# Performance work log

Measured on AMD Instinct MI355X. Metric: run time of the kernel, lower is better.

Reference implementation:

```python
import jax, jax.numpy as jnp
import numpy as np

B, N, H = 8, 2000, 64  # batch, num_nodes(=input_dim), hidden(num_gru_units)


def _laplacian_self_loop(a):
    # batched: norm = D^{-1/2} (A + I) D^{-1/2}
    m = a + jnp.eye(a.shape[-1], dtype=a.dtype)
    d_inv_sqrt = jnp.sum(m, axis=-1) ** -0.5  # (B, N)
    return d_inv_sqrt[..., :, None] * m * d_inv_sqrt[..., None, :]


def _graph_conv(inputs, hidden_flat, adj, windd, W2, b2, W3, b3, W, b, out_dim):
    b_, _, n = inputs.shape
    # dynamic wind-based adjacency
    wind_now = inputs[:, 2, :] * 360.0  # (B, N)
    direction = jnp.abs(windd[None, :, :] - wind_now[:, :, None])  # (B, N, N)
    direction = jnp.where(direction > 360.0, 180.0, direction)
    d1 = jnp.maximum(jnp.cos(direction * (jnp.pi / 180.0)), 0.0)
    a = d1 @ W2.T + b2 + (adj @ W3.T + b3)[None]  # (B, N, N)
    a1 = _laplacian_self_loop(jnp.maximum(a, 0.0))
    # graph conv: concat [x, h] then A @ [.] then Linear
    x = jnp.concatenate([inputs[:, 0, :, None], hidden_flat.reshape(b_, n, H)], axis=2)  # (B,N,H+1)
    y = jnp.einsum('bij,bjh->bih', a1, x) @ W.T + b  # (B, N, out_dim)
    return y.reshape(b_, n * out_dim)


def reference(inputs, hidden_state, adj, windd, W2, b2, W3, b3, W1a, b1a, W1b, b1b, Wca1, Wca2, Wsa):
    b_, _, n = inputs.shape
    conc = _graph_conv(inputs, hidden_state, adj, windd, W2, b2, W3, b3, W1a, b1a, 2 * H)
    conc = conc.reshape(b_, 2 * H, n)  # faithful reshape (input_dim == N)
    # --- channel attention (CBAM) ---
    avg = jnp.mean(conc, axis=2, keepdims=True)  # (B, 2H, 1)
    mx = jnp.max(conc, axis=2, keepdims=True)
    def fc(v):
        return jnp.einsum('oc,bcx->box', Wca2, jax.nn.relu(jnp.einsum('oc,bcx->box', Wca1, v)))
    ca = jax.nn.sigmoid(fc(avg) + fc(mx))  # (B, 2H, 1)
    conc = ca * conc
    # --- spatial attention ---
    s = jnp.stack([jnp.mean(conc, axis=1), jnp.max(conc, axis=1)], axis=1)  # (B, 2, N)
    sa = jax.lax.conv_general_dilated(s, Wsa, window_strides=(1,), padding=((3, 3),),
                                      dimension_numbers=('NCH', 'OIH', 'NCH'))  # (B,1,N)
    conc = jax.nn.sigmoid(sa) * conc
    # --- GRU gates ---
    conc = jax.nn.sigmoid(conc.reshape(b_, 2 * H * n))
    r, u = jnp.split(conc, 2, axis=1)  # each (B, N*H)
    c = jnp.tanh(_graph_conv(inputs, r * hidden_state, adj, windd, W2, b2, W3, b3, W1b, b1b, H))
    new_hidden_state = u * hidden_state + (1.0 - u) * c
    return new_hidden_state


def setup_inputs() -> dict:
    key = jax.random.key(0)
    ks = jax.random.split(key, 12)
    inputs = jax.random.uniform(ks[0], (B, 3, N), dtype=jnp.float32)
    hidden_state = jax.random.normal(ks[1], (B, N * H), dtype=jnp.float32) * 0.1
    adj = jax.random.uniform(ks[2], (N, N), dtype=jnp.float32)
    windd = jax.random.uniform(ks[3], (N, N), dtype=jnp.float32) * 360.0
    sN = 1.0 / np.sqrt(N)
    W2 = jax.random.normal(ks[4], (N, N), dtype=jnp.float32) * sN
    b2 = jnp.zeros((N,), jnp.float32)
    W3 = jax.random.normal(ks[5], (N, N), dtype=jnp.float32) * sN
    b3 = jnp.zeros((N,), jnp.float32)
    sI = 1.0 / np.sqrt(H + 1)
    W1a = jax.random.normal(ks[6], (2 * H, H + 1), dtype=jnp.float32) * sI
    b1a = jnp.ones((2 * H,), jnp.float32)  # bias=1.0 in graph_conv1
    W1b = jax.random.normal(ks[7], (H, H + 1), dtype=jnp.float32) * sI
    b1b = jnp.zeros((H,), jnp.float32)
    Wca1 = jax.random.normal(ks[8], (2 * H // 16, 2 * H), dtype=jnp.float32) * (1.0 / np.sqrt(2 * H))
    Wca2 = jax.random.normal(ks[9], (2 * H, 2 * H // 16), dtype=jnp.float32) * (1.0 / np.sqrt(2 * H // 16))
    Wsa = jax.random.normal(ks[10], (1, 2, 7), dtype=jnp.float32) * (1.0 / np.sqrt(14))
    return {'inputs': inputs, 'hidden_state': hidden_state, 'adj': adj, 'windd': windd,
            'W2': W2, 'b2': b2, 'W3': W3, 'b3': b3, 'W1a': W1a, 'b1a': b1a,
            'W1b': W1b, 'b1b': b1b, 'Wca1': Wca1, 'Wca2': Wca2, 'Wsa': Wsa}
```

## Files before the change

kernel.cpp:

```cpp
#include <hip/hip_runtime.h>

#define NN 2000
#define BB 8
#define P  2048
#define NIT 32

typedef __attribute__((ext_vector_type(8))) short bf16x8;
typedef __attribute__((ext_vector_type(4))) float f32x4;

__device__ __forceinline__ float sigf(float x) { return 1.0f / (1.0f + expf(-x)); }

__device__ __forceinline__ short f2bf(float x) {
    union { float f; unsigned u; } v; v.f = x;
    unsigned r = v.u + 0x7fffu + ((v.u >> 16) & 1u);
    return (short)(r >> 16);
}
__device__ __forceinline__ float bf2f(short h) {
    union { unsigned u; float f; } v; v.u = ((unsigned)(unsigned short)h) << 16; return v.f;
}

__device__ __forceinline__ void gl2lds16(const short* g, short* l) {
    __builtin_amdgcn_global_load_lds(
        (const __attribute__((address_space(1))) void*)g,
        (__attribute__((address_space(3))) void*)l, 16, 0, 0);
}

__global__ __launch_bounds__(256) void k_cvt(
    const float* __restrict__ W2, const float* __restrict__ W3,
    const float* __restrict__ adj, const float* __restrict__ windd,
    const float* __restrict__ inputs,
    short* __restrict__ W2bf, short* __restrict__ W3bf,
    short* __restrict__ adjbf, short* __restrict__ d1bf)
{
    const int i = blockIdx.x, sel = blockIdx.y, t = threadIdx.x;
    const bool live = (i < NN) && (t < 250);
    if (sel < 3) {
        const float* s = (sel == 0) ? W2 : (sel == 1) ? W3 : adj;
        short* d = ((sel == 0) ? W2bf : (sel == 1) ? W3bf : adjbf) + ((size_t)i) * P + t * 8;
        bf16x8 v;
#pragma unroll
        for (int e = 0; e < 8; ++e) v[e] = 0;
        if (live) {
            const float* p = s + (size_t)i * NN + t * 8;
            float4 x0 = *(const float4*)p;
            float4 x1 = *(const float4*)(p + 4);
            float a[8] = {x0.x,x0.y,x0.z,x0.w,x1.x,x1.y,x1.z,x1.w};
#pragma unroll
            for (int e = 0; e < 8; ++e) v[e] = f2bf(a[e]);
        }
        *(bf16x8*)d = v;
    } else {
        const float DEG = 0.01745329251994329577f;
        float cw[8], sw[8];
        if (live) {
            const float* p = windd + (size_t)i * NN + t * 8;
            float4 x0 = *(const float4*)p;
            float4 x1 = *(const float4*)(p + 4);
            float a[8] = {x0.x,x0.y,x0.z,x0.w,x1.x,x1.y,x1.z,x1.w};
#pragma unroll
            for (int e = 0; e < 8; ++e) {
                float r = a[e] * DEG;
                cw[e] = __cosf(r);
                sw[e] = __sinf(r);
            }
        }
        __shared__ float cwn[8], swn[8];
        if (t < 8 && i < NN) {
            float wn = inputs[(size_t)t * 3 * NN + 2 * NN + i] * (360.0f * DEG);
            cwn[t] = __cosf(wn);
            swn[t] = __sinf(wn);
        }
        __syncthreads();
#pragma unroll
        for (int b = 0; b < BB; ++b) {
            bf16x8 v;
#pragma unroll
            for (int e = 0; e < 8; ++e) v[e] = 0;
            if (live) {
                const float cb_ = cwn[b], sb_ = swn[b];
#pragma unroll
                for (int e = 0; e < 8; ++e)
                    v[e] = f2bf(fmaxf(fmaf(cw[e], cb_, sw[e] * sb_), 0.0f));
            }
            *(bf16x8*)(d1bf + ((size_t)b * P + i) * P + t * 8) = v;
        }
    }
}

__global__ __launch_bounds__(512, 2) void k_gd(
    const short* __restrict__ d1bf, const short* __restrict__ W2bf,
    const float* __restrict__ b2, const short* __restrict__ adjw,
    short* __restrict__ m_bf, float* __restrict__ rowpart)
{
    __shared__ char smem[131072];
    const int t = threadIdx.x;
    const int w = t >> 6, lane = t & 63;
    const int wm = w >> 2, wn = w & 3;
    const int lr = lane & 15, lq = lane >> 4;
    const int tile = blockIdx.x;
    const int b = blockIdx.y;
    const int i0 = (tile & 7) * 256;
    const int j0 = (tile >> 3) * 256;
    const short* A  = d1bf + (size_t)b * P * P;
    const short* Bm = W2bf;

    const short* srcA[4];
    const short* srcB[4];
#pragma unroll
    for (int q = 0; q < 4; ++q) {
        const int c = q * 512 + t;
        const int r = c >> 3;
        const int g = (c & 7) ^ (r & 7);
        srcA[q] = A  + (size_t)(i0 + r) * P + g * 8;
        srcB[q] = Bm + (size_t)(j0 + r) * P + g * 8;
    }

#define STAGE_ALL(slot, ktI) do {                                                      \
        gl2lds16(srcA[0] + (ktI) * 64, (short*)(smem + (slot) * 32768 + (w * 64) * 16));          \
        gl2lds16(srcA[1] + (ktI) * 64, (short*)(smem + (slot) * 32768 + (512 + w * 64) * 16));    \
        gl2lds16(srcA[2] + (ktI) * 64, (short*)(smem + (slot) * 32768 + (1024 + w * 64) * 16));   \
        gl2lds16(srcA[3] + (ktI) * 64, (short*)(smem + (slot) * 32768 + (1536 + w * 64) * 16));   \
        gl2lds16(srcB[0] + (ktI) * 64, (short*)(smem + 65536 + (slot) * 32768 + (w * 64) * 16));          \
        gl2lds16(srcB[1] + (ktI) * 64, (short*)(smem + 65536 + (slot) * 32768 + (512 + w * 64) * 16));    \
        gl2lds16(srcB[2] + (ktI) * 64, (short*)(smem + 65536 + (slot) * 32768 + (1024 + w * 64) * 16));   \
        gl2lds16(srcB[3] + (ktI) * 64, (short*)(smem + 65536 + (slot) * 32768 + (1536 + w * 64) * 16)); } while (0)

    const int fx0 = (lq << 4) ^ ((lr & 7) << 4);
    const int fx1 = ((4 + lq) << 4) ^ ((lr & 7) << 4);
    const int arowB = (wm * 128 + lr) * 128;
    const int browB = (wn * 64 + lr) * 128;

    f32x4 acc[8][4];
#pragma unroll
    for (int m = 0; m < 8; ++m)
#pragma unroll
        for (int n = 0; n < 4; ++n) acc[m][n] = (f32x4){0.f, 0.f, 0.f, 0.f};
    bf16x8 aF[4][2], bF[4][2];

    STAGE_ALL(0, 0);
    asm volatile("s_waitcnt vmcnt(0)" ::: "memory");
    __builtin_amdgcn_s_barrier();
    asm volatile("" ::: "memory");

#define MFMA_(a_, b_, m, n) acc[m][n] = __builtin_amdgcn_mfma_f32_16x16x32_bf16(a_, b_, acc[m][n], 0, 0, 0)

    for (int kt = 0; kt < NIT; ++kt) {
        char* curA = smem + (kt & 1) * 32768;
        char* curB = smem + 65536 + (kt & 1) * 32768;
        const int stgSlot = (kt + 1) & 1;
        const int stgKt = (kt + 1 < NIT) ? (kt + 1) : (NIT - 1);

        STAGE_ALL(stgSlot, stgKt);

#pragma unroll
        for (int m = 0; m < 4; ++m) {
            aF[m][0] = *(const bf16x8*)(curA + arowB + m * 2048 + fx0);
            aF[m][1] = *(const bf16x8*)(curA + arowB + m * 2048 + fx1);
        }
#pragma unroll
        for (int n = 0; n < 4; ++n) {
            bF[n][0] = *(const bf16x8*)(curB + browB + n * 2048 + fx0);
            bF[n][1] = *(const bf16x8*)(curB + browB + n * 2048 + fx1);
        }
        asm volatile("s_waitcnt lgkmcnt(0)" ::: "memory");
        __builtin_amdgcn_sched_barrier(0);
        __builtin_amdgcn_s_setprio(1);
#pragma unroll
        for (int m = 0; m < 4; ++m)
#pragma unroll
            for (int n = 0; n < 4; ++n) {
                MFMA_(aF[m][0], bF[n][0], m, n);
                MFMA_(aF[m][1], bF[n][1], m, n);
            }
        __builtin_amdgcn_s_setprio(0);

#pragma unroll
        for (int m = 0; m < 4; ++m) {
            aF[m][0] = *(const bf16x8*)(curA + arowB + (m + 4) * 2048 + fx0);
            aF[m][1] = *(const bf16x8*)(curA + arowB + (m + 4) * 2048 + fx1);
        }
        asm volatile("s_waitcnt lgkmcnt(0)" ::: "memory");
        __builtin_amdgcn_sched_barrier(0);
        __builtin_amdgcn_s_setprio(1);
#pragma unroll
        for (int m = 0; m < 4; ++m)
#pragma unroll
            for (int n = 0; n < 4; ++n) {
                MFMA_(aF[m][0], bF[n][0], m + 4, n);
                MFMA_(aF[m][1], bF[n][1], m + 4, n);
            }
        __builtin_amdgcn_s_setprio(0);

        asm volatile("s_waitcnt vmcnt(0)" ::: "memory");
        __builtin_amdgcn_s_barrier();
        asm volatile("" ::: "memory");
    }

    const int rbase = i0 + wm * 128 + lq * 4;
    const int cbase = j0 + wn * 64 + lr;
    float* red = (float*)smem;
#pragma unroll
    for (int m = 0; m < 8; ++m) {
#pragma unroll
        for (int q = 0; q < 4; ++q) {
            const int row = rbase + m * 16 + q;
            float rs = 0.0f;
#pragma unroll
            for (int n = 0; n < 4; ++n) {
                const int col = cbase + n * 16;
                short o = 0;
                if (row < NN && col < NN) {
                    float x = acc[m][n][q] + b2[col] + bf2f(adjw[(size_t)row * NN + col]);
                    x = fmaxf(x, 0.0f);
                    if (row == col) x += 1.0f;
                    o = f2bf(x);
                    rs += x;
                }
                m_bf[((size_t)b * P + row) * P + col] = o;
            }
            red[(wm * 128 + m * 16 + lq * 4 + q) * 66 + (wn * 16 + lr)] = rs;
        }
    }
    __syncthreads();
    if (t < 256) {
        const float* rr = red + t * 66;
        float s = 0.0f;
#pragma unroll
        for (int k2 = 0; k2 < 64; ++k2) s += rr[k2];
        const int row = i0 + t;
        if (row < NN)
            rowpart[((size_t)b * 8 + (tile >> 3)) * 2048 + row] = s;
    }
#undef MFMA_
#undef STAGE_ALL
}

template<int EPI>
__global__ __launch_bounds__(256) void k_mfma(
    const short* __restrict__ Abase, const short* __restrict__ Bbase,
    const float* __restrict__ bias,
    void* __restrict__ Cout, short* __restrict__ part, size_t aBatch)
{
    __shared__ short shA[4096];
    __shared__ short shB[4096];
    const int t = threadIdx.x;
    const int w = t >> 6, lane = t & 63;
    const int wr = w >> 1, wc = w & 1;

    int i0, j0, b, kt = 0;
    if (EPI == 2) {
        i0 = blockIdx.x * 128; j0 = 0; kt = blockIdx.y; b = blockIdx.z;
    } else {
        i0 = blockIdx.x * 128; j0 = blockIdx.y * 128; b = 0;
    }
    const int kb = (EPI == 2) ? kt * (P / 4) : 0;
    const int ke = (EPI == 2) ? kt * (P / 4) + (P / 4) : P;

    const short* A  = Abase + (size_t)b * aBatch;
    const short* Bm = Bbase + ((EPI == 2) ? (size_t)b * 128 * P : (size_t)0);

    f32x4 acc[4][4];
#pragma unroll
    for (int m = 0; m < 4; ++m)
#pragma unroll
        for (int n = 0; n < 4; ++n) acc[m][n] = (f32x4){0.f, 0.f, 0.f, 0.f};

    const int lidx0 = w * 128 + lane;
    const int lidx1 = lidx0 + 64;
    const int rA0 = lidx0 >> 2, rA1 = lidx1 >> 2;
    const int gA0 = (lidx0 & 3) ^ ((lidx0 >> 3) & 3);
    const int gA1 = (lidx1 & 3) ^ ((lidx1 >> 3) & 3);
    const short* aS0 = A  + (size_t)(i0 + rA0) * P + gA0 * 8;
    const short* aS1 = A  + (size_t)(i0 + rA1) * P + gA1 * 8;
    const short* bS0 = Bm + (size_t)(j0 + rA0) * P + gA0 * 8;
    const short* bS1 = Bm + (size_t)(j0 + rA1) * P + gA1 * 8;
    short* ldA0 = shA + lidx0 * 8 - lane * 8 + lane * 8;
    short* ldA1 = shA + lidx1 * 8;
    short* ldB0 = shB + lidx0 * 8;
    short* ldB1 = shB + lidx1 * 8;

    const int lr = lane & 15, lq = lane >> 4;
    const int axr = (lq ^ ((lr >> 1) & 3)) << 3;
    const int aoff = (wr * 64 + lr) * 32 + axr;
    const int boff = (wc * 64 + lr) * 32 + axr;

    for (int k0 = kb; k0 < ke; k0 += 32) {
        gl2lds16(aS0 + k0, ldA0);
        gl2lds16(aS1 + k0, ldA1);
        gl2lds16(bS0 + k0, ldB0);
        gl2lds16(bS1 + k0, ldB1);
        __syncthreads();
        bf16x8 aF[4], bF[4];
#pragma unroll
        for (int m = 0; m < 4; ++m) aF[m] = *(const bf16x8*)(shA + aoff + m * 512);
#pragma unroll
        for (int n = 0; n < 4; ++n) bF[n] = *(const bf16x8*)(shB + boff + n * 512);
#pragma unroll
        for (int m = 0; m < 4; ++m)
#pragma unroll
            for (int n = 0; n < 4; ++n)
                acc[m][n] = __builtin_amdgcn_mfma_f32_16x16x32_bf16(aF[m], bF[n], acc[m][n], 0, 0, 0);
        __syncthreads();
    }

    const int rbase = i0 + wr * 64 + lq * 4;
    const int cbase = j0 + wc * 64 + lr;
#pragma unroll
    for (int m = 0; m < 4; ++m) {
#pragma unroll
        for (int n = 0; n < 4; ++n) {
            const int col = cbase + n * 16;
#pragma unroll
            for (int q = 0; q < 4; ++q) {
                const int row = rbase + m * 16 + q;
                float v = acc[m][n][q];
                if (EPI == 0) {
                    if (row < NN && col < NN)
                        ((short*)Cout)[(size_t)row * NN + col] = f2bf(v + bias[col]);
                } else {
                    if (row < NN && col < 128)
                        part[((size_t)(kt * BB + b) * NN + row) * 128 + col] = f2bf(v);
                }
            }
        }
    }
}

__global__ __launch_bounds__(256) void k_agg64(
    const short* __restrict__ m_bf, const short* __restrict__ zT,
    short* __restrict__ part)
{
    __shared__ short shA[4096];
    __shared__ short shB[2048];
    const int t = threadIdx.x;
    const int w = t >> 6, lane = t & 63;
    const int wr = w >> 1, wc = w & 1;
    const int i0 = blockIdx.x * 128;
    const int kt = blockIdx.y, b = blockIdx.z;
    const int kb = kt * (P / 4), ke = kb + (P / 4);
    const short* A  = m_bf + (size_t)b * P * P;
    const short* Bm = zT + (size_t)b * 128 * P;

    f32x4 acc[4][2];
#pragma unroll
    for (int m = 0; m < 4; ++m)
#pragma unroll
        for (int n = 0; n < 2; ++n) acc[m][n] = (f32x4){0.f, 0.f, 0.f, 0.f};

    const int lidx0 = w * 128 + lane;
    const int lidx1 = lidx0 + 64;
    const int gA0 = (lidx0 & 3) ^ ((lidx0 >> 3) & 3);
    const int gA1 = (lidx1 & 3) ^ ((lidx1 >> 3) & 3);
    const int gB  = (t & 3) ^ ((t >> 3) & 3);
    const short* aS0 = A  + (size_t)(i0 + (lidx0 >> 2)) * P + gA0 * 8;
    const short* aS1 = A  + (size_t)(i0 + (lidx1 >> 2)) * P + gA1 * 8;
    const short* bS  = Bm + (size_t)(t >> 2) * P + gB * 8;
    short* ldA0 = shA + lidx0 * 8;
    short* ldA1 = shA + lidx1 * 8;
    short* ldB  = shB + t * 8;

    const int lr = lane & 15, lq = lane >> 4;
    const int axr = (lq ^ ((lr >> 1) & 3)) << 3;
    const int aoff = (wr * 64 + lr) * 32 + axr;
    const int boff = (wc * 32 + lr) * 32 + axr;

    for (int k0 = kb; k0 < ke; k0 += 32) {
        gl2lds16(aS0 + k0, ldA0);
        gl2lds16(aS1 + k0, ldA1);
        gl2lds16(bS + k0, ldB);
        __syncthreads();
        bf16x8 aF[4], bF[2];
#pragma unroll
        for (int m = 0; m < 4; ++m) aF[m] = *(const bf16x8*)(shA + aoff + m * 512);
#pragma unroll
        for (int n = 0; n < 2; ++n) bF[n] = *(const bf16x8*)(shB + boff + n * 512);
#pragma unroll
        for (int m = 0; m < 4; ++m)
#pragma unroll
            for (int n = 0; n < 2; ++n)
                acc[m][n] = __builtin_amdgcn_mfma_f32_16x16x32_bf16(aF[m], bF[n], acc[m][n], 0, 0, 0);
        __syncthreads();
    }

    const int rbase = i0 + wr * 64 + lq * 4;
    const int cbase = wc * 32 + lr;
#pragma unroll
    for (int m = 0; m < 4; ++m) {
#pragma unroll
        for (int n = 0; n < 2; ++n) {
            const int col = cbase + n * 16;
#pragma unroll
            for (int q = 0; q < 4; ++q) {
                const int row = rbase + m * 16 + q;
                if (row < NN)
                    part[((size_t)(kt * BB + b) * NN + row) * 64 + col] = f2bf(acc[m][n][q]);
            }
        }
    }
}

__global__ __launch_bounds__(256) void k_combred(
    const short* __restrict__ part, const float* __restrict__ dinv,
    const float* __restrict__ bias, float* __restrict__ conc,
    float* __restrict__ avg, float* __restrict__ mx)
{
    const int c = blockIdx.x, b = blockIdx.y, t = threadIdx.x;
    const size_t S = (size_t)BB * NN * 128;
    const size_t base = (size_t)b * NN * 128;
    float sm = 0.0f, sx = -3.402823466e+38f;
    for (int n = t; n < NN; n += 256) {
        const size_t f = (size_t)c * NN + n;
        const int i = (int)(f >> 7), o = (int)(f & 127);
        const size_t pidx = base + f;
        float s = (bf2f(part[pidx]) + bf2f(part[pidx + S])) +
                  (bf2f(part[pidx + 2 * S]) + bf2f(part[pidx + 3 * S]));
        float v = s * dinv[b * NN + i] + bias[o];
        conc[pidx] = v;
        sm += v; sx = fmaxf(sx, v);
    }
#pragma unroll
    for (int off = 32; off > 0; off >>= 1) {
        sm += __shfl_down(sm, off);
        sx = fmaxf(sx, __shfl_down(sx, off));
    }
    __shared__ float rs[4], rm[4];
    if ((t & 63) == 0) { rs[t >> 6] = sm; rm[t >> 6] = sx; }
    __syncthreads();
    if (t == 0) {
        avg[b * 128 + c] = (rs[0] + rs[1] + rs[2] + rs[3]) * (1.0f / NN);
        mx[b * 128 + c]  = fmaxf(fmaxf(rm[0], rm[1]), fmaxf(rm[2], rm[3]));
    }
}

__global__ __launch_bounds__(256) void k_cfin(
    const short* __restrict__ part, const float* __restrict__ dinv,
    const float* __restrict__ bias, const float* __restrict__ u,
    const float* __restrict__ hidden, float* __restrict__ out)
{
    const size_t idx = (size_t)blockIdx.x * 256 + threadIdx.x;
    const size_t S = (size_t)BB * NN * 64;
    if (idx >= S) return;
    const int o = (int)(idx & 63);
    const size_t r = idx >> 6;
    const int i = (int)(r % NN);
    const int b = (int)(r / NN);
    float s = (bf2f(part[idx]) + bf2f(part[idx + S])) +
              (bf2f(part[idx + 2 * S]) + bf2f(part[idx + 3 * S]));
    float c = tanhf(s * dinv[b * NN + i] + bias[o]);
    float uu = u[idx];
    out[idx] = uu * hidden[idx] + (1.0f - uu) * c;
}

template<int OUT>
__global__ __launch_bounds__(128) void k_xwT(
    const float* __restrict__ inputs, const float* __restrict__ hsrc,
    const float* __restrict__ W, const float* __restrict__ rowpart,
    float* __restrict__ dinv, short* __restrict__ zT)
{
    const int b = blockIdx.y;
    const int j0 = blockIdx.x * 16;
    const int t = threadIdx.x;
    __shared__ float wl[128 * 65];
    __shared__ float xs[16 * 66];
    __shared__ float dj[16];
    for (int idx = t; idx < OUT * 65; idx += 128) wl[idx] = W[idx];
    for (int idx = t; idx < 16 * 64; idx += 128) {
        int jj = idx >> 6, hh = idx & 63, j = j0 + jj;
        xs[jj * 66 + 1 + hh] = (j < NN) ? hsrc[((size_t)b * NN + j) * 64 + hh] : 0.0f;
    }
    if (t < 16) {
        int j = j0 + t;
        xs[t * 66] = (j < NN) ? inputs[(size_t)b * 3 * NN + j] : 0.0f;
        float dv = 0.0f;
        if (j < NN) {
            if (OUT == 128) {
                float s = 0.0f;
#pragma unroll
                for (int jt = 0; jt < 8; ++jt)
                    s += rowpart[((size_t)b * 8 + jt) * 2048 + j];
                dv = rsqrtf(s);
                dinv[b * NN + j] = dv;
            } else {
                dv = dinv[b * NN + j];
            }
        }
        dj[t] = dv;
    }
    __syncthreads();
    for (int jj = 0; jj < 16; ++jj) {
        float a = 0.0f;
        if (t < OUT) {
            const float* xr = &xs[jj * 66];
            const float* wr = &wl[t * 65];
#pragma unroll
            for (int c = 0; c < 65; ++c) a = fmaf(xr[c], wr[c], a);
        }
        int j = j0 + jj;
        zT[((size_t)b * 128 + t) * P + j] = (t < OUT && j < NN) ? f2bf(a * dj[jj]) : (short)0;
    }
}

__global__ __launch_bounds__(256) void k_satgate(
    const float* __restrict__ conc, const float* __restrict__ avg,
    const float* __restrict__ mxv, const float* __restrict__ Wca1,
    const float* __restrict__ Wca2, const float* __restrict__ Wsa,
    const float* __restrict__ hidden, float* __restrict__ rh, float* __restrict__ u)
{
    const int b = blockIdx.y;
    const int n0 = blockIdx.x * 256;
    const int t = threadIdx.x;
    __shared__ float av[128], mv[128], h[16], cas[128];
    __shared__ float wsa[14];
    __shared__ float s0l[262], s1l[262];
    if (t < 128) { av[t] = avg[b * 128 + t]; mv[t] = mxv[b * 128 + t]; }
    if (t >= 128 && t < 142) wsa[t - 128] = Wsa[t - 128];
    __syncthreads();
    if (t < 16) {
        int o8 = t & 7;
        const float* src = (t < 8) ? av : mv;
        float s = 0.0f;
        for (int c = 0; c < 128; ++c) s = fmaf(Wca1[o8 * 128 + c], src[c], s);
        h[t] = fmaxf(s, 0.0f);
    }
    __syncthreads();
    if (t < 128) {
        float s = 0.0f;
#pragma unroll
        for (int k = 0; k < 8; ++k) s = fmaf(Wca2[t * 8 + k], h[k] + h[8 + k], s);
        cas[t] = sigf(s);
    }
    __syncthreads();

    const float* cb = conc + (size_t)b * NN * 128;
    {
        const int n = n0 + t;
        float sm = 0.0f, sx = -3.402823466e+38f;
        if (n < NN) {
            for (int c = 0; c < 128; ++c) {
                float v = cas[c] * cb[(size_t)c * NN + n];
                sm += v; sx = fmaxf(sx, v);
            }
            s0l[t + 3] = sm * (1.0f / 128.0f);
            s1l[t + 3] = sx;
        } else { s0l[t + 3] = 0.0f; s1l[t + 3] = 0.0f; }
    }
    if (t < 6) {
        const int hn = (t < 3) ? (n0 - 3 + t) : (n0 + 256 + (t - 3));
        const int hi = (t < 3) ? t : (256 + t);
        float sm = 0.0f, sx = -3.402823466e+38f;
        if (hn >= 0 && hn < NN) {
            for (int c = 0; c < 128; ++c) {
                float v = cas[c] * cb[(size_t)c * NN + hn];
                sm += v; sx = fmaxf(sx, v);
            }
            s0l[hi] = sm * (1.0f / 128.0f);
            s1l[hi] = sx;
        } else { s0l[hi] = 0.0f; s1l[hi] = 0.0f; }
    }
    __syncthreads();

    const int n = n0 + t;
    if (n >= NN) return;
    float sa = 0.0f;
#pragma unroll
    for (int k = 0; k < 7; ++k)
        sa += wsa[k] * s0l[t + k] + wsa[7 + k] * s1l[t + k];
    float gs = sigf(sa);
    for (int c = 0; c < 128; ++c) {
        float v = gs * cas[c] * cb[(size_t)c * NN + n];
        float g = sigf(v);
        if (c < 64)
            rh[(size_t)b * NN * 64 + (size_t)c * NN + n] =
                g * hidden[(size_t)b * NN * 64 + (size_t)c * NN + n];
        else
            u[(size_t)b * NN * 64 + (size_t)(c - 64) * NN + n] = g;
    }
}

extern "C" void kernel_launch(void* const* d_in, const int* in_sizes, int n_in,
                              void* d_out, int out_size, void* d_ws, size_t ws_size,
                              hipStream_t stream)
{
    (void)in_sizes; (void)n_in; (void)out_size; (void)ws_size;
    const float* inputs = (const float*)d_in[0];
    const float* hidden = (const float*)d_in[1];
    const float* adj    = (const float*)d_in[2];
    const float* windd  = (const float*)d_in[3];
    const float* W2     = (const float*)d_in[4];
    const float* b2     = (const float*)d_in[5];
    const float* W3     = (const float*)d_in[6];
    const float* b3     = (const float*)d_in[7];
    const float* W1a    = (const float*)d_in[8];
    const float* b1a    = (const float*)d_in[9];
    const float* W1b    = (const float*)d_in[10];
    const float* b1b    = (const float*)d_in[11];
    const float* Wca1   = (const float*)d_in[12];
    const float* Wca2   = (const float*)d_in[13];
    const float* Wsa    = (const float*)d_in[14];
    float* out = (float*)d_out;

    char* W = (char*)d_ws;
    short* adjW3bf = (short*)(W + 0);
    short* W2bf    = (short*)(W + 8000000);
    short* W3bf    = (short*)(W + 16388608);
    short* adjbf   = (short*)(W + 24777216);
    short* m_bf    = (short*)(W + 16388608);
    char* D = W + 83497472;
    short* d1bf = (short*)D;
    float* dinv = (float*)(D + 0);
    float* avgb = (float*)(D + 64000);
    float* mxb  = (float*)(D + 68096);
    short* zT   = (short*)(D + 204800);
    float* conc = (float*)(D + 4399104);
    float* rh   = (float*)(D + 12591104);
    float* ubuf = (float*)(D + 16687104);
    short* part = (short*)(D + 24879104);
    float* rowpart = (float*)(D + 67108864);

    const size_t PP = (size_t)P * P;

    k_cvt<<<dim3(P, 4), 256, 0, stream>>>(W2, W3, adj, windd, inputs,
                                          W2bf, W3bf, adjbf, d1bf);
    k_mfma<0><<<dim3(16, 16, 1), 256, 0, stream>>>(adjbf, W3bf, b3, adjW3bf, nullptr, 0);
    k_gd<<<dim3(64, BB), 512, 0, stream>>>(d1bf, W2bf, b2, adjW3bf, m_bf, rowpart);
    k_xwT<128><<<dim3(128, BB), 128, 0, stream>>>(inputs, hidden, W1a, rowpart, dinv, zT);
    k_mfma<2><<<dim3(16, 4, BB), 256, 0, stream>>>(m_bf, zT, nullptr, nullptr, part, PP);
    k_combred<<<dim3(128, BB), 256, 0, stream>>>(part, dinv, b1a, conc, avgb, mxb);
    k_satgate<<<dim3(8, BB), 256, 0, stream>>>(conc, avgb, mxb, Wca1, Wca2, Wsa, hidden, rh, ubuf);
    k_xwT<64><<<dim3(128, BB), 128, 0, stream>>>(inputs, rh, W1b, rowpart, dinv, zT);
    k_agg64<<<dim3(16, 4, BB), 256, 0, stream>>>(m_bf, zT, part);
    k_cfin<<<(BB * NN * 64 + 255) / 256, 256, 0, stream>>>(part, dinv, b1b, ubuf, hidden, out);
}
```

Baseline: 388.0 us.

## Shrink main GEMM tiles to 128x128 and store conc activations as bf16

```diff
diff --git a/kernel.cpp b/kernel.cpp
--- a/kernel.cpp
+++ b/kernel.cpp
@@ -3,7 +3,7 @@
 #define NN 2000
 #define BB 8
 #define P  2048
-#define NIT 32
+#define NI2 64
 
 typedef __attribute__((ext_vector_type(8))) short bf16x8;
 typedef __attribute__((ext_vector_type(4))) float f32x4;
@@ -87,108 +87,75 @@
     }
 }
 
-__global__ __launch_bounds__(512, 2) void k_gd(
+__global__ __launch_bounds__(256, 3) void k_g2b(
     const short* __restrict__ d1bf, const short* __restrict__ W2bf,
     const float* __restrict__ b2, const short* __restrict__ adjw,
     short* __restrict__ m_bf, float* __restrict__ rowpart)
 {
-    __shared__ char smem[131072];
+    __shared__ char smem[32768];
     const int t = threadIdx.x;
     const int w = t >> 6, lane = t & 63;
-    const int wm = w >> 2, wn = w & 3;
+    const int wm = w >> 1, wn = w & 1;
     const int lr = lane & 15, lq = lane >> 4;
     const int tile = blockIdx.x;
     const int b = blockIdx.y;
-    const int i0 = (tile & 7) * 256;
-    const int j0 = (tile >> 3) * 256;
+    const int i0 = (tile & 15) * 128;
+    const int j0 = (tile >> 4) * 128;
     const short* A  = d1bf + (size_t)b * P * P;
     const short* Bm = W2bf;
 
-    const short* srcA[4];
-    const short* srcB[4];
-#pragma unroll
-    for (int q = 0; q < 4; ++q) {
-        const int c = q * 512 + t;
-        const int r = c >> 3;
-        const int g = (c & 7) ^ (r & 7);
+    const short* srcA[2];
+    const short* srcB[2];
+    int dstO[2];
+#pragma unroll
+    for (int q = 0; q < 2; ++q) {
+        const int c = q * 256 + t;
+        const int r = c >> 2;
+        const int g = (c & 3) ^ ((r >> 1) & 3);
         srcA[q] = A  + (size_t)(i0 + r) * P + g * 8;
         srcB[q] = Bm + (size_t)(j0 + r) * P + g * 8;
-    }
-
-#define STAGE_ALL(slot, ktI) do {                                                      \
-        gl2lds16(srcA[0] + (ktI) * 64, (short*)(smem + (slot) * 32768 + (w * 64) * 16));          \
-        gl2lds16(srcA[1] + (ktI) * 64, (short*)(smem + (slot) * 32768 + (512 + w * 64) * 16));    \
-        gl2lds16(srcA[2] + (ktI) * 64, (short*)(smem + (slot) * 32768 + (1024 + w * 64) * 16));   \
-        gl2lds16(srcA[3] + (ktI) * 64, (short*)(smem + (slot) * 32768 + (1536 + w * 64) * 16));   \
-        gl2lds16(srcB[0] + (ktI) * 64, (short*)(smem + 65536 + (slot) * 32768 + (w * 64) * 16));          \
-        gl2lds16(srcB[1] + (ktI) * 64, (short*)(smem + 65536 + (slot) * 32768 + (512 + w * 64) * 16));    \
-        gl2lds16(srcB[2] + (ktI) * 64, (short*)(smem + 65536 + (slot) * 32768 + (1024 + w * 64) * 16));   \
-        gl2lds16(srcB[3] + (ktI) * 64, (short*)(smem + 65536 + (slot) * 32768 + (1536 + w * 64) * 16)); } while (0)
-
-    const int fx0 = (lq << 4) ^ ((lr & 7) << 4);
-    const int fx1 = ((4 + lq) << 4) ^ ((lr & 7) << 4);
-    const int arowB = (wm * 128 + lr) * 128;
-    const int browB = (wn * 64 + lr) * 128;
-
-    f32x4 acc[8][4];
-#pragma unroll
-    for (int m = 0; m < 8; ++m)
+        dstO[q] = c * 16;
+    }
+
+#define STG(slot, ktI) do {                                                            \
+        gl2lds16(srcA[0] + (ktI) * 32, (short*)(smem + (slot) * 16384 + dstO[0]));     \
+        gl2lds16(srcA[1] + (ktI) * 32, (short*)(smem + (slot) * 16384 + dstO[1]));     \
+        gl2lds16(srcB[0] + (ktI) * 32, (short*)(smem + (slot) * 16384 + 8192 + dstO[0])); \
+        gl2lds16(srcB[1] + (ktI) * 32, (short*)(smem + (slot) * 16384 + 8192 + dstO[1])); } while (0)
+
+    const int fx = (lq ^ ((lr >> 1) & 3)) << 4;
+    const int arowB = (wm * 64 + lr) * 64;
+    const int browB = 8192 + (wn * 64 + lr) * 64;
+
+    f32x4 acc[4][4];
+#pragma unroll
+    for (int m = 0; m < 4; ++m)
 #pragma unroll
         for (int n = 0; n < 4; ++n) acc[m][n] = (f32x4){0.f, 0.f, 0.f, 0.f};
-    bf16x8 aF[4][2], bF[4][2];
-
-    STAGE_ALL(0, 0);
+
+    STG(0, 0);
     asm volatile("s_waitcnt vmcnt(0)" ::: "memory");
     __builtin_amdgcn_s_barrier();
     asm volatile("" ::: "memory");
 
-#define MFMA_(a_, b_, m, n) acc[m][n] = __builtin_amdgcn_mfma_f32_16x16x32_bf16(a_, b_, acc[m][n], 0, 0, 0)
-
-    for (int kt = 0; kt < NIT; ++kt) {
-        char* curA = smem + (kt & 1) * 32768;
-        char* curB = smem + 65536 + (kt & 1) * 32768;
-        const int stgSlot = (kt + 1) & 1;
-        const int stgKt = (kt + 1 < NIT) ? (kt + 1) : (NIT - 1);
-
-        STAGE_ALL(stgSlot, stgKt);
-
-#pragma unroll
-        for (int m = 0; m < 4; ++m) {
-            aF[m][0] = *(const bf16x8*)(curA + arowB + m * 2048 + fx0);
-            aF[m][1] = *(const bf16x8*)(curA + arowB + m * 2048 + fx1);
-        }
-#pragma unroll
-        for (int n = 0; n < 4; ++n) {
-            bF[n][0] = *(const bf16x8*)(curB + browB + n * 2048 + fx0);
-            bF[n][1] = *(const bf16x8*)(curB + browB + n * 2048 + fx1);
-        }
+    for (int kt = 0; kt < NI2; ++kt) {
+        char* cur = smem + (kt & 1) * 16384;
+        const int stgKt = (kt + 1 < NI2) ? (kt + 1) : (NI2 - 1);
+        STG((kt + 1) & 1, stgKt);
+
+        bf16x8 aF[4], bF[4];
+#pragma unroll
+        for (int m = 0; m < 4; ++m) aF[m] = *(const bf16x8*)(cur + arowB + m * 1024 + fx);
+#pragma unroll
+        for (int n = 0; n < 4; ++n) bF[n] = *(const bf16x8*)(cur + browB + n * 1024 + fx);
         asm volatile("s_waitcnt lgkmcnt(0)" ::: "memory");
         __builtin_amdgcn_sched_barrier(0);
         __builtin_amdgcn_s_setprio(1);
 #pragma unroll
         for (int m = 0; m < 4; ++m)
 #pragma unroll
-            for (int n = 0; n < 4; ++n) {
-                MFMA_(aF[m][0], bF[n][0], m, n);
-                MFMA_(aF[m][1], bF[n][1], m, n);
-            }
-        __builtin_amdgcn_s_setprio(0);
-
-#pragma unroll
-        for (int m = 0; m < 4; ++m) {
-            aF[m][0] = *(const bf16x8*)(curA + arowB + (m + 4) * 2048 + fx0);
-            aF[m][1] = *(const bf16x8*)(curA + arowB + (m + 4) * 2048 + fx1);
-        }
-        asm volatile("s_waitcnt lgkmcnt(0)" ::: "memory");
-        __builtin_amdgcn_sched_barrier(0);
-        __builtin_amdgcn_s_setprio(1);
-#pragma unroll
-        for (int m = 0; m < 4; ++m)
-#pragma unroll
-            for (int n = 0; n < 4; ++n) {
-                MFMA_(aF[m][0], bF[n][0], m + 4, n);
-                MFMA_(aF[m][1], bF[n][1], m + 4, n);
-            }
+            for (int n = 0; n < 4; ++n)
+                acc[m][n] = __builtin_amdgcn_mfma_f32_16x16x32_bf16(aF[m], bF[n], acc[m][n], 0, 0, 0);
         __builtin_amdgcn_s_setprio(0);
 
         asm volatile("s_waitcnt vmcnt(0)" ::: "memory");
@@ -196,11 +163,11 @@
         asm volatile("" ::: "memory");
     }
 
-    const int rbase = i0 + wm * 128 + lq * 4;
+    const int rbase = i0 + wm * 64 + lq * 4;
     const int cbase = j0 + wn * 64 + lr;
     float* red = (float*)smem;
 #pragma unroll
-    for (int m = 0; m < 8; ++m) {
+    for (int m = 0; m < 4; ++m) {
 #pragma unroll
         for (int q = 0; q < 4; ++q) {
             const int row = rbase + m * 16 + q;
@@ -218,21 +185,20 @@
                 }
                 m_bf[((size_t)b * P + row) * P + col] = o;
             }
-            red[(wm * 128 + m * 16 + lq * 4 + q) * 66 + (wn * 16 + lr)] = rs;
-        }
-    }
-    __syncthreads();
-    if (t < 256) {
-        const float* rr = red + t * 66;
+            red[(wm * 64 + m * 16 + lq * 4 + q) * 34 + (wn * 16 + lr)] = rs;
+        }
+    }
+    __syncthreads();
+    if (t < 128) {
+        const float* rr = red + t * 34;
         float s = 0.0f;
 #pragma unroll
-        for (int k2 = 0; k2 < 64; ++k2) s += rr[k2];
+        for (int k2 = 0; k2 < 32; ++k2) s += rr[k2];
         const int row = i0 + t;
         if (row < NN)
-            rowpart[((size_t)b * 8 + (tile >> 3)) * 2048 + row] = s;
-    }
-#undef MFMA_
-#undef STAGE_ALL
+            rowpart[((size_t)b * 16 + (tile >> 4)) * 2048 + row] = s;
+    }
+#undef STG
 }
 
 template<int EPI>
@@ -267,14 +233,13 @@
 
     const int lidx0 = w * 128 + lane;
     const int lidx1 = lidx0 + 64;
-    const int rA0 = lidx0 >> 2, rA1 = lidx1 >> 2;
     const int gA0 = (lidx0 & 3) ^ ((lidx0 >> 3) & 3);
     const int gA1 = (lidx1 & 3) ^ ((lidx1 >> 3) & 3);
-    const short* aS0 = A  + (size_t)(i0 + rA0) * P + gA0 * 8;
-    const short* aS1 = A  + (size_t)(i0 + rA1) * P + gA1 * 8;
-    const short* bS0 = Bm + (size_t)(j0 + rA0) * P + gA0 * 8;
-    const short* bS1 = Bm + (size_t)(j0 + rA1) * P + gA1 * 8;
-    short* ldA0 = shA + lidx0 * 8 - lane * 8 + lane * 8;
+    const short* aS0 = A  + (size_t)(i0 + (lidx0 >> 2)) * P + gA0 * 8;
+    const short* aS1 = A  + (size_t)(i0 + (lidx1 >> 2)) * P + gA1 * 8;
+    const short* bS0 = Bm + (size_t)(j0 + (lidx0 >> 2)) * P + gA0 * 8;
+    const short* bS1 = Bm + (size_t)(j0 + (lidx1 >> 2)) * P + gA1 * 8;
+    short* ldA0 = shA + lidx0 * 8;
     short* ldA1 = shA + lidx1 * 8;
     short* ldB0 = shB + lidx0 * 8;
     short* ldB1 = shB + lidx1 * 8;
@@ -401,7 +366,7 @@
 
 __global__ __launch_bounds__(256) void k_combred(
     const short* __restrict__ part, const float* __restrict__ dinv,
-    const float* __restrict__ bias, float* __restrict__ conc,
+    const float* __restrict__ bias, short* __restrict__ conc,
     float* __restrict__ avg, float* __restrict__ mx)
 {
     const int c = blockIdx.x, b = blockIdx.y, t = threadIdx.x;
@@ -415,7 +380,7 @@
         float s = (bf2f(part[pidx]) + bf2f(part[pidx + S])) +
                   (bf2f(part[pidx + 2 * S]) + bf2f(part[pidx + 3 * S]));
         float v = s * dinv[b * NN + i] + bias[o];
-        conc[pidx] = v;
+        conc[pidx] = f2bf(v);
         sm += v; sx = fmaxf(sx, v);
     }
 #pragma unroll
@@ -476,8 +441,8 @@
             if (OUT == 128) {
                 float s = 0.0f;
 #pragma unroll
-                for (int jt = 0; jt < 8; ++jt)
-                    s += rowpart[((size_t)b * 8 + jt) * 2048 + j];
+                for (int jt = 0; jt < 16; ++jt)
+                    s += rowpart[((size_t)b * 16 + jt) * 2048 + j];
                 dv = rsqrtf(s);
                 dinv[b * NN + j] = dv;
             } else {
@@ -501,7 +466,7 @@
 }
 
 __global__ __launch_bounds__(256) void k_satgate(
-    const float* __restrict__ conc, const float* __restrict__ avg,
+    const short* __restrict__ conc, const float* __restrict__ avg,
     const float* __restrict__ mxv, const float* __restrict__ Wca1,
     const float* __restrict__ Wca2, const float* __restrict__ Wsa,
     const float* __restrict__ hidden, float* __restrict__ rh, float* __restrict__ u)
@@ -531,13 +496,13 @@
     }
     __syncthreads();
 
-    const float* cb = conc + (size_t)b * NN * 128;
+    const short* cb = conc + (size_t)b * NN * 128;
     {
         const int n = n0 + t;
         float sm = 0.0f, sx = -3.402823466e+38f;
         if (n < NN) {
             for (int c = 0; c < 128; ++c) {
-                float v = cas[c] * cb[(size_t)c * NN + n];
+                float v = cas[c] * bf2f(cb[(size_t)c * NN + n]);
                 sm += v; sx = fmaxf(sx, v);
             }
             s0l[t + 3] = sm * (1.0f / 128.0f);
@@ -550,7 +515,7 @@
         float sm = 0.0f, sx = -3.402823466e+38f;
         if (hn >= 0 && hn < NN) {
             for (int c = 0; c < 128; ++c) {
-                float v = cas[c] * cb[(size_t)c * NN + hn];
+                float v = cas[c] * bf2f(cb[(size_t)c * NN + hn]);
                 sm += v; sx = fmaxf(sx, v);
             }
             s0l[hi] = sm * (1.0f / 128.0f);
@@ -567,7 +532,7 @@
         sa += wsa[k] * s0l[t + k] + wsa[7 + k] * s1l[t + k];
     float gs = sigf(sa);
     for (int c = 0; c < 128; ++c) {
-        float v = gs * cas[c] * cb[(size_t)c * NN + n];
+        float v = gs * cas[c] * bf2f(cb[(size_t)c * NN + n]);
         float g = sigf(v);
         if (c < 64)
             rh[(size_t)b * NN * 64 + (size_t)c * NN + n] =
@@ -611,7 +576,7 @@
     float* avgb = (float*)(D + 64000);
     float* mxb  = (float*)(D + 68096);
     short* zT   = (short*)(D + 204800);
-    float* conc = (float*)(D + 4399104);
+    short* conc = (short*)(D + 4399104);
     float* rh   = (float*)(D + 12591104);
     float* ubuf = (float*)(D + 16687104);
     short* part = (short*)(D + 24879104);
@@ -622,7 +587,7 @@
     k_cvt<<<dim3(P, 4), 256, 0, stream>>>(W2, W3, adj, windd, inputs,
                                           W2bf, W3bf, adjbf, d1bf);
     k_mfma<0><<<dim3(16, 16, 1), 256, 0, stream>>>(adjbf, W3bf, b3, adjW3bf, nullptr, 0);
-    k_gd<<<dim3(64, BB), 512, 0, stream>>>(d1bf, W2bf, b2, adjW3bf, m_bf, rowpart);
+    k_g2b<<<dim3(256, BB), 256, 0, stream>>>(d1bf, W2bf, b2, adjW3bf, m_bf, rowpart);
     k_xwT<128><<<dim3(128, BB), 128, 0, stream>>>(inputs, hidden, W1a, rowpart, dinv, zT);
     k_mfma<2><<<dim3(16, 4, BB), 256, 0, stream>>>(m_bf, zT, nullptr, nullptr, part, PP);
     k_combred<<<dim3(128, BB), 256, 0, stream>>>(part, dinv, b1a, conc, avgb, mxb);
```

After: 410.4 us. 1.06x slower.
